# Kernel tuning notes

Measured on AMD Instinct MI355X. Metric: run time of the kernel, lower is better.

## Reference

```python
import jax, jax.numpy as jnp
import numpy as np

NUM_HEADS = 12
EPS = 1e-4


def softmax_kernel(data, proj, is_query):
    # data: [B,H,N,d], proj: [M,d] -> phi: [B,H,N,M]  (Performer softmax-kernel features)
    d = data.shape[-1]
    data_normalizer = d ** -0.25
    ratio = proj.shape[0] ** -0.5
    data_dash = jnp.einsum('bhnd,md->bhnm', data_normalizer * data, proj)
    diag = jnp.sum(data * data, axis=-1, keepdims=True) * 0.5 * (data_normalizer ** 2)
    if is_query:
        m = jnp.max(data_dash, axis=-1, keepdims=True)
    else:
        m = jnp.max(data_dash, axis=(-3, -2, -1), keepdims=True)
    return ratio * (jnp.exp(data_dash - diag - m) + EPS)


def setup_inputs() -> dict:
    key = jax.random.key(0)
    ks = jax.random.split(key, 5)
    B, N, C = 8, 4096, 768
    x = jax.random.normal(ks[0], (B, N, C), dtype=jnp.float32)
    w_qkv = jax.random.normal(ks[1], (3 * C, C), dtype=jnp.float32) * 0.02
    w_proj = jax.random.normal(ks[2], (C, C), dtype=jnp.float32) * 0.02
    b_proj = jnp.zeros((C,), dtype=jnp.float32)
    proj_mat = jax.random.normal(ks[3], (256, C // NUM_HEADS), dtype=jnp.float32)
    return {"x": x, "w_qkv": w_qkv, "w_proj": w_proj, "b_proj": b_proj, "proj_mat": proj_mat}


def reference(x, w_qkv, w_proj, b_proj, proj_mat):
    B, N, C = x.shape
    H = NUM_HEADS
    d = C // H
    qkv = (x @ w_qkv.T).reshape(B, N, 3, H, d).transpose(2, 0, 3, 1, 4)  # [3,B,H,N,d]
    q, k, v = qkv[0], qkv[1], qkv[2]
    q_prime = softmax_kernel(q, proj_mat, is_query=True)   # [B,H,N,M]
    k_prime = softmax_kernel(k, proj_mat, is_query=False)  # [B,H,N,M]
    # non-causal linear attention: out = phi(q) (phi(k)^T v) / (phi(q) sum phi(k))
    k_sum = jnp.sum(k_prime, axis=-2)                       # [B,H,M]
    d_inv = 1.0 / jnp.einsum('bhnm,bhm->bhn', q_prime, k_sum)
    context = jnp.einsum('bhnm,bhnd->bhmd', k_prime, v)     # [B,H,M,d]
    out = jnp.einsum('bhnm,bhmd,bhn->bhnd', q_prime, context, d_inv)
    out = out.transpose(0, 2, 1, 3).reshape(B, N, C)        # b h n d -> b n (h d)
    return out @ w_proj.T + b_proj
```

## Files before the change

kernel.cpp:

```cpp
#include <hip/hip_runtime.h>
#include <hip/hip_bf16.h>

typedef __attribute__((ext_vector_type(4))) float f32x4;
typedef __attribute__((ext_vector_type(8))) short s16x8;
typedef __attribute__((ext_vector_type(4))) float f4v;
typedef __attribute__((ext_vector_type(4))) unsigned short us4;
typedef unsigned short u16;
typedef unsigned int u32;

#define H_ 12
#define NTOK 4096
#define DHEAD 64
#define MFEAT 256
#define CDIM 768

#define NORMALIZER 0.35355339059327373f
#define DIAGSCALE 0.0625f
#define RATIO_ 0.0625f
#define EPS_ 1e-4f
#define DEFER_THR 4.0f

#define MFMA(a, b, c) __builtin_amdgcn_mfma_f32_16x16x32_bf16((a), (b), (c), 0, 0, 0)

__device__ __forceinline__ float bf2f(u16 u) {
  union { float f; u32 v; } x; x.v = ((u32)u) << 16; return x.f;
}
__device__ __forceinline__ u16 f2bf(float f) {
  union { float f; u32 v; } x; x.f = f;
  u32 v = x.v + 0x7FFFu + ((x.v >> 16) & 1u);
  return (u16)(v >> 16);
}
__device__ __forceinline__ u32 fenc(float f) {
  u32 u = __float_as_uint(f);
  return (u & 0x80000000u) ? ~u : (u | 0x80000000u);
}
__device__ __forceinline__ float fdec(u32 k) {
  u32 u = (k & 0x80000000u) ? (k & 0x7fffffffu) : ~k;
  return __uint_as_float(u);
}
__device__ __forceinline__ void glds16(const u16* g, u16* l) {
  __builtin_amdgcn_global_load_lds((const __attribute__((address_space(1))) void*)g,
                                   (__attribute__((address_space(3))) void*)l, 16, 0, 0);
}

__device__ __forceinline__ void st_write64(const u16* stw, u16* dst, long ld, int lane) {
  int r0 = lane >> 3, cc = lane & 7;
#pragma unroll
  for (int c = 0; c < 8; ++c) {
    int row = c * 8 + r0;
    s16x8 v = *(const s16x8*)(stw + row * 72 + cc * 8);
    *(s16x8*)(dst + (long)row * ld + cc * 8) = v;
  }
}

__global__ void cvt_all(const float* __restrict__ x, const float* __restrict__ wq,
                        const float* __restrict__ wp, const float* __restrict__ pj,
                        u16* __restrict__ xb, u16* __restrict__ wqb,
                        u16* __restrict__ wpb, u16* __restrict__ pjb, u32* __restrict__ mk) {
  int b = blockIdx.x;
  if (b == 0 && threadIdx.x < 8) mk[threadIdx.x] = 0u;
  const float* s;
  u16* d;
  int base;
  if (b < 24576)      { s = x;  d = xb;  base = b; }
  else if (b < 26304) { s = wq; d = wqb; base = b - 24576; }
  else if (b < 26880) { s = wp; d = wpb; base = b - 26304; }
  else                { s = pj; d = pjb; base = b - 26880; }
  long i = (long)base * 256 + threadIdx.x;
  f4v v = *(const f4v*)(s + i * 4);
  us4 o;
#pragma unroll
  for (int j = 0; j < 4; ++j) o[j] = f2bf(v[j]);
  *(us4*)(d + i * 4) = o;
}

__global__ __launch_bounds__(256) void k0_qkv(const u16* __restrict__ A, const u16* __restrict__ Bm,
                                              const u16* __restrict__ projb,
                                              u16* __restrict__ qb, u16* __restrict__ kb,
                                              u16* __restrict__ vT, u32* __restrict__ mk) {
  __shared__ u16 smem[4 * 64 * 72];
  u16* lA = smem;
  u16* lB = smem + 8192;
  int tid = threadIdx.x, lane = tid & 63, wid = tid >> 6;
  int p = blockIdx.x + blockIdx.y * 18;
  int r8 = p & 7, q = p >> 3;
  int bx = q % 18;
  int by = (q / 18) * 8 + r8;
  int m0 = by << 7, n0 = bx << 7;
  int wr = (wid >> 1) << 6, wc = (wid & 1) << 6;
  int l15 = lane & 15, lk = lane >> 4;
  int lr = lane >> 3;
  int lu = (lane & 7) ^ lr;
  const u16* Ab = A + (long)m0 * CDIM;
  const u16* Bb = Bm + (long)n0 * CDIM;
  const u16* gA = Ab + (long)(wid * 32 + lr) * CDIM + lu * 8;
  const u16* gB = Bb + (long)(wid * 32 + lr) * CDIM + lu * 8;
  u16* dA = lA + wid * 2048;
  u16* dB = lB + wid * 2048;
  f32x4 acc[4][4];
#pragma unroll
  for (int i = 0; i < 4; ++i)
#pragma unroll
    for (int j = 0; j < 4; ++j) acc[i][j] = (f32x4){0.f, 0.f, 0.f, 0.f};
  for (int k0 = 0; k0 < CDIM; k0 += 64) {
    __syncthreads();
#pragma unroll
    for (int g = 0; g < 4; ++g) {
      glds16(gA + k0 + (long)g * 8 * CDIM, dA + g * 512);
      glds16(gB + k0 + (long)g * 8 * CDIM, dB + g * 512);
    }
    __syncthreads();
#pragma unroll
    for (int ks = 0; ks < 2; ++ks) {
      s16x8 af[4], bv[4];
#pragma unroll
      for (int i = 0; i < 4; ++i) {
        int co = ((ks * 4 + lk) ^ (l15 & 7)) * 8;
        af[i] = *(const s16x8*)(lA + (wr + i * 16 + l15) * 64 + co);
        bv[i] = *(const s16x8*)(lB + (wc + i * 16 + l15) * 64 + co);
      }
#pragma unroll
      for (int i = 0; i < 4; ++i)
#pragma unroll
        for (int j = 0; j < 4; ++j) acc[i][j] = MFMA(af[i], bv[j], acc[i][j]);
    }
  }
  __syncthreads();
  int colbase = n0 + wc;
  int qi = colbase / CDIM;
  int h = (colbase % CDIM) >> 6;
  int rowbase = m0 + wr;
  int b = rowbase >> 12;
  int nloc = rowbase & (NTOK - 1);
  u16* stw = smem + wid * 4608;
  if (qi < 2) {
#pragma unroll
    for (int i = 0; i < 4; ++i)
#pragma unroll
      for (int j = 0; j < 4; ++j)
#pragma unroll
        for (int r = 0; r < 4; ++r)
          stw[(i * 16 + lk * 4 + r) * 72 + j * 16 + l15] = f2bf(acc[i][j][r]);
    u16* dst = (qi == 0 ? qb : kb) + ((long)(b * H_ + h) * NTOK + nloc) * DHEAD;
    st_write64(stw, dst, DHEAD, lane);
    if (qi == 1) {
      float wm = -3.4e38f;
#pragma unroll
      for (int jc = 0; jc < 8; ++jc) {
        s16x8 af2[4][2], bv2[2][2];
#pragma unroll
        for (int ks = 0; ks < 2; ++ks) {
#pragma unroll
          for (int i = 0; i < 4; ++i)
            af2[i][ks] = *(const s16x8*)(stw + (i * 16 + l15) * 72 + ks * 32 + lk * 8);
#pragma unroll
          for (int j2 = 0; j2 < 2; ++j2)
            bv2[j2][ks] = *(const s16x8*)(projb + (long)(jc * 32 + j2 * 16 + l15) * DHEAD + ks * 32 + lk * 8);
        }
        f32x4 dacc[4][2];
#pragma unroll
        for (int i = 0; i < 4; ++i)
#pragma unroll
          for (int j2 = 0; j2 < 2; ++j2) dacc[i][j2] = (f32x4){0.f, 0.f, 0.f, 0.f};
#pragma unroll
        for (int ks = 0; ks < 2; ++ks)
#pragma unroll
          for (int i = 0; i < 4; ++i)
#pragma unroll
            for (int j2 = 0; j2 < 2; ++j2)
              dacc[i][j2] = MFMA(af2[i][ks], bv2[j2][ks], dacc[i][j2]);
#pragma unroll
        for (int i = 0; i < 4; ++i)
#pragma unroll
          for (int j2 = 0; j2 < 2; ++j2)
#pragma unroll
            for (int r = 0; r < 4; ++r) wm = fmaxf(wm, dacc[i][j2][r]);
      }
      wm = fmaxf(wm, __shfl_xor(wm, 1));
      wm = fmaxf(wm, __shfl_xor(wm, 2));
      wm = fmaxf(wm, __shfl_xor(wm, 4));
      wm = fmaxf(wm, __shfl_xor(wm, 8));
      wm = fmaxf(wm, __shfl_xor(wm, 16));
      wm = fmaxf(wm, __shfl_xor(wm, 32));
      if (lane == 0) atomicMax(mk + b, fenc(wm * NORMALIZER));
    }
  } else {
#pragma unroll
    for (int i = 0; i < 4; ++i)
#pragma unroll
      for (int j = 0; j < 4; ++j) {
        us4 w;
#pragma unroll
        for (int r = 0; r < 4; ++r) w[r] = f2bf(acc[i][j][r]);
        *(us4*)(stw + (j * 16 + l15) * 72 + i * 16 + lk * 4) = w;
      }
    u16* dst = vT + (long)(b * H_ + h) * DHEAD * NTOK + nloc;
    st_write64(stw, dst, NTOK, lane);
  }
}

__global__ __launch_bounds__(256) void k3f(const u16* __restrict__ kb, const u16* __restrict__ vT,
                                           const u16* __restrict__ projb, const u32* __restrict__ mk,
                                           float* __restrict__ ctx8, float* __restrict__ kpart) {
  __shared__ u16 smem[4 * 64 * 72];
  int bh = blockIdx.y, nc = blockIdx.x;
  int tid = threadIdx.x, lane = tid & 63, wid = tid >> 6;
  int l15 = lane & 15, lk = lane >> 4;
  int wc = wid << 6;
  float mg = fdec(mk[bh / H_]);
  const u16* Kb = kb + ((long)bh * NTOK + nc * 512) * DHEAD;
  const u16* Vb = vT + (long)bh * DHEAD * NTOK + nc * 512;
  u16* ktw = smem + wid * 4608;
  f32x4 ctxa[4][4];
#pragma unroll
  for (int i = 0; i < 4; ++i)
#pragma unroll
    for (int j = 0; j < 4; ++j) ctxa[i][j] = (f32x4){0.f, 0.f, 0.f, 0.f};
  float cs[4] = {0.f, 0.f, 0.f, 0.f};
  for (int sb = 0; sb < 8; ++sb) {
    const u16* Ksb = Kb + sb * 64 * DHEAD;
    s16x8 a[4][2];
    float ss[4] = {0.f, 0.f, 0.f, 0.f};
#pragma unroll
    for (int i = 0; i < 4; ++i)
#pragma unroll
      for (int ks = 0; ks < 2; ++ks) {
        a[i][ks] = *(const s16x8*)(Ksb + (long)(i * 16 + l15) * DHEAD + ks * 32 + lk * 8);
#pragma unroll
        for (int e = 0; e < 8; ++e) { float f = bf2f((u16)a[i][ks][e]); ss[i] += f * f; }
      }
    float dgv[4];
#pragma unroll
    for (int i = 0; i < 4; ++i) {
      float s = ss[i];
      s += __shfl_xor(s, 16);
      s += __shfl_xor(s, 32);
      dgv[i] = s * DIAGSCALE;
    }
    f32x4 dacc[4][4];
#pragma unroll
    for (int i = 0; i < 4; ++i)
#pragma unroll
      for (int j = 0; j < 4; ++j) dacc[i][j] = (f32x4){0.f, 0.f, 0.f, 0.f};
    __builtin_amdgcn_s_setprio(1);
#pragma unroll
    for (int ks = 0; ks < 2; ++ks)
#pragma unroll
      for (int j = 0; j < 4; ++j) {
        s16x8 pb = *(const s16x8*)(projb + (long)(wc + j * 16 + l15) * DHEAD + ks * 32 + lk * 8);
#pragma unroll
        for (int i = 0; i < 4; ++i) dacc[i][j] = MFMA(a[i][ks], pb, dacc[i][j]);
      }
    __builtin_amdgcn_s_setprio(0);
    float dgr[4][4];
#pragma unroll
    for (int i = 0; i < 4; ++i)
#pragma unroll
      for (int r = 0; r < 4; ++r) dgr[i][r] = __shfl(dgv[i], 4 * lk + r);
#pragma unroll
    for (int i = 0; i < 4; ++i)
#pragma unroll
      for (int j = 0; j < 4; ++j) {
        us4 w;
#pragma unroll
        for (int r = 0; r < 4; ++r) {
          float v = RATIO_ * (__expf(dacc[i][j][r] * NORMALIZER - dgr[i][r] - mg) + EPS_);
          cs[j] += v;
          w[r] = f2bf(v);
        }
        *(us4*)(ktw + (j * 16 + l15) * 72 + i * 16 + lk * 4) = w;
      }
    __builtin_amdgcn_s_setprio(1);
#pragma unroll
    for (int ks = 0; ks < 2; ++ks) {
      s16x8 a2f[4], vb[4];
#pragma unroll
      for (int ii = 0; ii < 4; ++ii)
        a2f[ii] = *(const s16x8*)(ktw + (ii * 16 + l15) * 72 + ks * 32 + lk * 8);
#pragma unroll
      for (int jv = 0; jv < 4; ++jv)
        vb[jv] = *(const s16x8*)(Vb + (long)(jv * 16 + l15) * NTOK + sb * 64 + ks * 32 + lk * 8);
#pragma unroll
      for (int ii = 0; ii < 4; ++ii)
#pragma unroll
        for (int jv = 0; jv < 4; ++jv) ctxa[ii][jv] = MFMA(a2f[ii], vb[jv], ctxa[ii][jv]);
    }
    __builtin_amdgcn_s_setprio(0);
  }
  asm volatile("" ::: "memory");
  float* lf = (float*)ktw;
  float* dstb = ctx8 + (long)(nc * 96 + bh) * (MFEAT * DHEAD);
#pragma unroll
  for (int half = 0; half < 2; ++half) {
#pragma unroll
    for (int jh = 0; jh < 2; ++jh) {
      int jv = half * 2 + jh;
#pragma unroll
      for (int ii = 0; ii < 4; ++ii)
        *(f4v*)(lf + (jh * 16 + l15) * 68 + ii * 16 + lk * 4) =
            (f4v){ctxa[ii][jv][0], ctxa[ii][jv][1], ctxa[ii][jv][2], ctxa[ii][jv][3]};
    }
#pragma unroll
    for (int u = 0; u < 8; ++u) {
      int dd_l = u * 4 + lk;
      f4v v = *(const f4v*)(lf + dd_l * 68 + l15 * 4);
      *(f4v*)(dstb + (long)(half * 32 + dd_l) * MFEAT + wc + l15 * 4) = v;
    }
    asm volatile("" ::: "memory");
  }
#pragma unroll
  for (int j = 0; j < 4; ++j) {
    float s = cs[j];
    s += __shfl_xor(s, 16);
    s += __shfl_xor(s, 32);
    if (lk == 0) kpart[((long)bh * 8 + nc) * MFEAT + wc + j * 16 + l15] = s;
  }
}

__global__ __launch_bounds__(256) void k3b(const float* __restrict__ ctx8, const float* __restrict__ kpart,
                                           u16* __restrict__ baug, float* __restrict__ bsum) {
  int bh = blockIdx.x, y = blockIdx.y;
  int tid = threadIdx.x;
  u16* o = baug + (long)bh * 80 * MFEAT;
  if (y < 4) {
    int dd = y * 16 + (tid >> 4);
    int m0 = (tid & 15) * 16;
    f4v s[4];
#pragma unroll
    for (int e = 0; e < 4; ++e) s[e] = (f4v){0.f, 0.f, 0.f, 0.f};
    for (int c = 0; c < 8; ++c) {
      const float* r = ctx8 + (long)(c * 96 + bh) * (MFEAT * DHEAD) + dd * MFEAT + m0;
#pragma unroll
      for (int e = 0; e < 4; ++e) s[e] += *(const f4v*)(r + e * 4);
    }
    float t = 0.f;
#pragma unroll
    for (int e = 0; e < 4; ++e) {
      us4 w;
#pragma unroll
      for (int q = 0; q < 4; ++q) { t += s[e][q]; w[q] = f2bf(s[e][q]); }
      *(us4*)(o + dd * MFEAT + m0 + e * 4) = w;
    }
    t += __shfl_xor(t, 1); t += __shfl_xor(t, 2); t += __shfl_xor(t, 4); t += __shfl_xor(t, 8);
    if ((tid & 15) == 0) bsum[bh * 80 + dd] = t;
  } else {
    __shared__ float red[4];
    int m = tid;
    float ks = 0.f;
    for (int c = 0; c < 8; ++c) ks += kpart[((long)bh * 8 + c) * MFEAT + m];
    o[64 * MFEAT + m] = f2bf(ks);
    float t = ks;
    t += __shfl_xor(t, 1); t += __shfl_xor(t, 2); t += __shfl_xor(t, 4);
    t += __shfl_xor(t, 8); t += __shfl_xor(t, 16); t += __shfl_xor(t, 32);
    if ((m & 63) == 0) red[m >> 6] = t;
    __syncthreads();
    if (m == 0) bsum[bh * 80 + 64] = red[0] + red[1] + red[2] + red[3];
    for (int dd = 65; dd < 80; ++dd) o[dd * MFEAT + m] = 0;
    if (m < 15) bsum[bh * 80 + 65 + m] = 0.f;
  }
}

__global__ __launch_bounds__(256) void k2q5(const u16* __restrict__ qb, const u16* __restrict__ projb,
                                            const u16* __restrict__ baug, const float* __restrict__ bsum,
                                            u16* __restrict__ attn) {
  __shared__ u16 smem[4 * 64 * 72];
  int bh = blockIdx.y;
  int b = bh / H_, h = bh % H_;
  int tid = threadIdx.x, lane = tid & 63, wid = tid >> 6;
  int l15 = lane & 15, lk = lane >> 4;
  int tb = blockIdx.x * 256 + wid * 64;
  const u16* Aq = qb + ((long)bh * NTOK + tb) * DHEAD;
  const u16* Bb = baug + (long)bh * 80 * MFEAT;
  u16* qTw = smem + wid * 4608;

  s16x8 a2[4][2];
  float ssv[4] = {0.f, 0.f, 0.f, 0.f};
#pragma unroll
  for (int i = 0; i < 4; ++i)
#pragma unroll
    for (int ks = 0; ks < 2; ++ks) {
      a2[i][ks] = *(const s16x8*)(Aq + (long)(i * 16 + l15) * DHEAD + ks * 32 + lk * 8);
#pragma unroll
      for (int e = 0; e < 8; ++e) { float f = bf2f((u16)a2[i][ks][e]); ssv[i] += f * f; }
    }
  float dgv[4];
#pragma unroll
  for (int i = 0; i < 4; ++i) {
    float s = ssv[i];
    s += __shfl_xor(s, 16);
    s += __shfl_xor(s, 32);
    dgv[i] = s * DIAGSCALE;
  }
  float rm[4] = {-3.4e38f, -3.4e38f, -3.4e38f, -3.4e38f};
  float tm[4] = {-3.4e38f, -3.4e38f, -3.4e38f, -3.4e38f};
  f32x4 oacc[5][4];
#pragma unroll
  for (int jo = 0; jo < 5; ++jo)
#pragma unroll
    for (int i = 0; i < 4; ++i) oacc[jo][i] = (f32x4){0.f, 0.f, 0.f, 0.f};

  for (int c = 0; c < 8; ++c) {
    s16x8 pb[2][2];
#pragma unroll
    for (int j = 0; j < 2; ++j)
#pragma unroll
      for (int ks = 0; ks < 2; ++ks)
        pb[j][ks] = *(const s16x8*)(projb + (long)(c * 32 + j * 16 + l15) * DHEAD + ks * 32 + lk * 8);
    f32x4 dacc[2][4];
#pragma unroll
    for (int j = 0; j < 2; ++j)
#pragma unroll
      for (int i = 0; i < 4; ++i) dacc[j][i] = (f32x4){0.f, 0.f, 0.f, 0.f};
    __builtin_amdgcn_s_setprio(1);
#pragma unroll
    for (int ks = 0; ks < 2; ++ks)
#pragma unroll
      for (int j = 0; j < 2; ++j)
#pragma unroll
        for (int i = 0; i < 4; ++i) dacc[j][i] = MFMA(pb[j][ks], a2[i][ks], dacc[j][i]);
    __builtin_amdgcn_s_setprio(0);
#pragma unroll
    for (int i = 0; i < 4; ++i) {
      float cm = dacc[0][i][0];
      cm = fmaxf(cm, dacc[0][i][1]); cm = fmaxf(cm, dacc[0][i][2]); cm = fmaxf(cm, dacc[0][i][3]);
      cm = fmaxf(cm, dacc[1][i][0]); cm = fmaxf(cm, dacc[1][i][1]);
      cm = fmaxf(cm, dacc[1][i][2]); cm = fmaxf(cm, dacc[1][i][3]);
      cm = fmaxf(cm, __shfl_xor(cm, 16));
      cm = fmaxf(cm, __shfl_xor(cm, 32));
      tm[i] = fmaxf(tm[i], cm);
      if (__any((cm - rm[i]) * NORMALIZER > DEFER_THR)) {
        float rn = fmaxf(rm[i], cm);
        float fsc = __expf((rm[i] - rn) * NORMALIZER);
#pragma unroll
        for (int jo = 0; jo < 5; ++jo) oacc[jo][i] *= fsc;
        rm[i] = rn;
      }
    }
#pragma unroll
    for (int i = 0; i < 4; ++i) {
      float dm = dgv[i] + rm[i] * NORMALIZER;
#pragma unroll
      for (int j = 0; j < 2; ++j) {
        us4 w;
#pragma unroll
        for (int r = 0; r < 4; ++r)
          w[r] = f2bf(RATIO_ * __expf(dacc[j][i][r] * NORMALIZER - dm));
        *(us4*)(qTw + (i * 16 + l15) * 40 + j * 16 + lk * 4) = w;
      }
    }
    s16x8 bB[5], qf[4];
#pragma unroll
    for (int jo = 0; jo < 5; ++jo)
      bB[jo] = *(const s16x8*)(Bb + (long)(jo * 16 + l15) * MFEAT + c * 32 + lk * 8);
#pragma unroll
    for (int i = 0; i < 4; ++i)
      qf[i] = *(const s16x8*)(qTw + (i * 16 + l15) * 40 + lk * 8);
    __builtin_amdgcn_s_setprio(1);
#pragma unroll
    for (int jo = 0; jo < 5; ++jo)
#pragma unroll
      for (int i = 0; i < 4; ++i) oacc[jo][i] = MFMA(bB[jo], qf[i], oacc[jo][i]);
    __builtin_amdgcn_s_setprio(0);
  }
  float lamv[4];
#pragma unroll
  for (int i = 0; i < 4; ++i) lamv[i] = __expf((tm[i] - rm[i]) * NORMALIZER);
#pragma unroll
  for (int jo = 0; jo < 5; ++jo) {
    f4v bs = *(const f4v*)(bsum + (long)bh * 80 + jo * 16 + lk * 4);
#pragma unroll
    for (int i = 0; i < 4; ++i)
#pragma unroll
      for (int r = 0; r < 4; ++r) oacc[jo][i][r] += (RATIO_ * EPS_) * bs[r] * lamv[i];
  }
  u16* stw = qTw;
#pragma unroll
  for (int i = 0; i < 4; ++i) {
    float dn = __shfl(oacc[4][i][0], l15);
    float inv = 1.0f / dn;
#pragma unroll
    for (int jo = 0; jo < 4; ++jo) {
      us4 w;
#pragma unroll
      for (int r = 0; r < 4; ++r) w[r] = f2bf(oacc[jo][i][r] * inv);
      *(us4*)(stw + (i * 16 + l15) * 72 + jo * 16 + lk * 4) = w;
    }
  }
  u16* dst = attn + ((long)b * NTOK + tb) * CDIM + h * DHEAD;
  st_write64(stw, dst, CDIM, lane);
}

__global__ __launch_bounds__(256) void k6_proj(const u16* __restrict__ A, const u16* __restrict__ Bm,
                                               const float* __restrict__ bproj, float* __restrict__ out) {
  __shared__ u16 smem[16384];
  u16* lA = smem;
  u16* lB = smem + 8192;
  int tid = threadIdx.x, lane = tid & 63, wid = tid >> 6;
  int p = blockIdx.x + blockIdx.y * 6;
  int r8 = p & 7, q = p >> 3;
  int bx = q % 6;
  int by = (q / 6) * 8 + r8;
  int m0 = by << 7, n0 = bx << 7;
  int wr = (wid >> 1) << 6, wc = (wid & 1) << 6;
  int l15 = lane & 15, lk = lane >> 4;
  int lr = lane >> 3;
  int lu = (lane & 7) ^ lr;
  const u16* Ab = A + (long)m0 * CDIM;
  const u16* Bb = Bm + (long)n0 * CDIM;
  const u16* gA = Ab + (long)(wid * 32 + lr) * CDIM + lu * 8;
  const u16* gB = Bb + (long)(wid * 32 + lr) * CDIM + lu * 8;
  u16* dA = lA + wid * 2048;
  u16* dB = lB + wid * 2048;
  f32x4 acc[4][4];
#pragma unroll
  for (int i = 0; i < 4; ++i)
#pragma unroll
    for (int j = 0; j < 4; ++j) acc[i][j] = (f32x4){0.f, 0.f, 0.f, 0.f};
  for (int k0 = 0; k0 < CDIM; k0 += 64) {
    __syncthreads();
#pragma unroll
    for (int g = 0; g < 4; ++g) {
      glds16(gA + k0 + (long)g * 8 * CDIM, dA + g * 512);
      glds16(gB + k0 + (long)g * 8 * CDIM, dB + g * 512);
    }
    __syncthreads();
#pragma unroll
    for (int ks = 0; ks < 2; ++ks) {
      s16x8 af[4], bv[4];
#pragma unroll
      for (int i = 0; i < 4; ++i) {
        int co = ((ks * 4 + lk) ^ (l15 & 7)) * 8;
        af[i] = *(const s16x8*)(lA + (wr + i * 16 + l15) * 64 + co);
        bv[i] = *(const s16x8*)(lB + (wc + i * 16 + l15) * 64 + co);
      }
#pragma unroll
      for (int i = 0; i < 4; ++i)
#pragma unroll
        for (int j = 0; j < 4; ++j) acc[i][j] = MFMA(af[i], bv[j], acc[i][j]);
    }
  }
  float bpv[4];
#pragma unroll
  for (int j = 0; j < 4; ++j) bpv[j] = bproj[n0 + wc + j * 16 + l15];
#pragma unroll
  for (int i = 0; i < 4; ++i)
#pragma unroll
    for (int j = 0; j < 4; ++j)
#pragma unroll
      for (int r = 0; r < 4; ++r) {
        long row = m0 + wr + i * 16 + lk * 4 + r;
        int col = n0 + wc + j * 16 + l15;
        out[row * CDIM + col] = acc[i][j][r] + bpv[j];
      }
}

extern "C" void kernel_launch(void* const* d_in, const int* in_sizes, int n_in,
                              void* d_out, int out_size, void* d_ws, size_t ws_size,
                              hipStream_t stream) {
  const float* x = (const float*)d_in[0];
  const float* w_qkv = (const float*)d_in[1];
  const float* w_proj = (const float*)d_in[2];
  const float* b_proj = (const float*)d_in[3];
  const float* proj = (const float*)d_in[4];
  float* out = (float*)d_out;

  char* p = (char*)d_ws;
  auto take = [&](size_t bytes) {
    char* r = p;
    p += (bytes + 255) & ~(size_t)255;
    return r;
  };
  u16* xb = (u16*)take(32768UL * 768 * 2);
  u16* wqkvb = (u16*)take(2304UL * 768 * 2);
  u16* wprojb = (u16*)take(768UL * 768 * 2);
  u16* projb = (u16*)take(256UL * 64 * 2);
  u16* qb = (u16*)take(96UL * 4096 * 64 * 2);
  u16* kb = (u16*)take(96UL * 4096 * 64 * 2);
  u16* vT = (u16*)take(96UL * 64 * 4096 * 2);
  float* kpart = (float*)take(96UL * 8 * 256 * 4);
  u32* mk = (u32*)take(256);
  u16* baug = (u16*)take(96UL * 80 * 256 * 2);
  float* bsum = (float*)take(96UL * 80 * 4);
  float* ctx8 = (float*)xb;
  u16* attn = kb;

  cvt_all<<<26896, 256, 0, stream>>>(x, w_qkv, w_proj, proj, xb, wqkvb, wprojb, projb, mk);
  k0_qkv<<<dim3(18, 256), 256, 0, stream>>>(xb, wqkvb, projb, qb, kb, vT, mk);
  k3f<<<dim3(8, 96), 256, 0, stream>>>(kb, vT, projb, mk, ctx8, kpart);
  k3b<<<dim3(96, 5), 256, 0, stream>>>(ctx8, kpart, baug, bsum);
  k2q5<<<dim3(16, 96), 256, 0, stream>>>(qb, projb, baug, bsum, attn);
  k6_proj<<<dim3(6, 256), 256, 0, stream>>>(attn, wprojb, b_proj, out);
}
```

Baseline: 455.9 us.

## Replace global key-max prepass with online per-wave running max and rescaling

Drops the extra projection GEMM and atomicMax that k0_qkv ran on K to find the global per-batch max. k3f now keeps a running max per wave, rescaling its partial context and key sums only when the max jumps past a threshold. It also records per-chunk maxima and V column sums. k3b recombines the partials with exp scale factors and adds the EPS term analytically through the V sums. This removes redundant MFMA work and the atomic from the QKV GEMM epilogue, at the cost of extra reduction logic, more buffers, and possible numeric drift when a rescale is deferred.

```diff
diff --git a/kernel.cpp b/kernel.cpp
--- a/kernel.cpp
+++ b/kernel.cpp
@@ -30,14 +30,6 @@
   u32 v = x.v + 0x7FFFu + ((x.v >> 16) & 1u);
   return (u16)(v >> 16);
 }
-__device__ __forceinline__ u32 fenc(float f) {
-  u32 u = __float_as_uint(f);
-  return (u & 0x80000000u) ? ~u : (u | 0x80000000u);
-}
-__device__ __forceinline__ float fdec(u32 k) {
-  u32 u = (k & 0x80000000u) ? (k & 0x7fffffffu) : ~k;
-  return __uint_as_float(u);
-}
 __device__ __forceinline__ void glds16(const u16* g, u16* l) {
   __builtin_amdgcn_global_load_lds((const __attribute__((address_space(1))) void*)g,
                                    (__attribute__((address_space(3))) void*)l, 16, 0, 0);
@@ -56,9 +48,8 @@
 __global__ void cvt_all(const float* __restrict__ x, const float* __restrict__ wq,
                         const float* __restrict__ wp, const float* __restrict__ pj,
                         u16* __restrict__ xb, u16* __restrict__ wqb,
-                        u16* __restrict__ wpb, u16* __restrict__ pjb, u32* __restrict__ mk) {
+                        u16* __restrict__ wpb, u16* __restrict__ pjb) {
   int b = blockIdx.x;
-  if (b == 0 && threadIdx.x < 8) mk[threadIdx.x] = 0u;
   const float* s;
   u16* d;
   int base;
@@ -75,9 +66,8 @@
 }
 
 __global__ __launch_bounds__(256) void k0_qkv(const u16* __restrict__ A, const u16* __restrict__ Bm,
-                                              const u16* __restrict__ projb,
                                               u16* __restrict__ qb, u16* __restrict__ kb,
-                                              u16* __restrict__ vT, u32* __restrict__ mk) {
+                                              u16* __restrict__ vT) {
   __shared__ u16 smem[4 * 64 * 72];
   u16* lA = smem;
   u16* lB = smem + 8192;
@@ -143,47 +133,6 @@
           stw[(i * 16 + lk * 4 + r) * 72 + j * 16 + l15] = f2bf(acc[i][j][r]);
     u16* dst = (qi == 0 ? qb : kb) + ((long)(b * H_ + h) * NTOK + nloc) * DHEAD;
     st_write64(stw, dst, DHEAD, lane);
-    if (qi == 1) {
-      float wm = -3.4e38f;
-#pragma unroll
-      for (int jc = 0; jc < 8; ++jc) {
-        s16x8 af2[4][2], bv2[2][2];
-#pragma unroll
-        for (int ks = 0; ks < 2; ++ks) {
-#pragma unroll
-          for (int i = 0; i < 4; ++i)
-            af2[i][ks] = *(const s16x8*)(stw + (i * 16 + l15) * 72 + ks * 32 + lk * 8);
-#pragma unroll
-          for (int j2 = 0; j2 < 2; ++j2)
-            bv2[j2][ks] = *(const s16x8*)(projb + (long)(jc * 32 + j2 * 16 + l15) * DHEAD + ks * 32 + lk * 8);
-        }
-        f32x4 dacc[4][2];
-#pragma unroll
-        for (int i = 0; i < 4; ++i)
-#pragma unroll
-          for (int j2 = 0; j2 < 2; ++j2) dacc[i][j2] = (f32x4){0.f, 0.f, 0.f, 0.f};
-#pragma unroll
-        for (int ks = 0; ks < 2; ++ks)
-#pragma unroll
-          for (int i = 0; i < 4; ++i)
-#pragma unroll
-            for (int j2 = 0; j2 < 2; ++j2)
-              dacc[i][j2] = MFMA(af2[i][ks], bv2[j2][ks], dacc[i][j2]);
-#pragma unroll
-        for (int i = 0; i < 4; ++i)
-#pragma unroll
-          for (int j2 = 0; j2 < 2; ++j2)
-#pragma unroll
-            for (int r = 0; r < 4; ++r) wm = fmaxf(wm, dacc[i][j2][r]);
-      }
-      wm = fmaxf(wm, __shfl_xor(wm, 1));
-      wm = fmaxf(wm, __shfl_xor(wm, 2));
-      wm = fmaxf(wm, __shfl_xor(wm, 4));
-      wm = fmaxf(wm, __shfl_xor(wm, 8));
-      wm = fmaxf(wm, __shfl_xor(wm, 16));
-      wm = fmaxf(wm, __shfl_xor(wm, 32));
-      if (lane == 0) atomicMax(mk + b, fenc(wm * NORMALIZER));
-    }
   } else {
 #pragma unroll
     for (int i = 0; i < 4; ++i)
@@ -200,14 +149,15 @@
 }
 
 __global__ __launch_bounds__(256) void k3f(const u16* __restrict__ kb, const u16* __restrict__ vT,
-                                           const u16* __restrict__ projb, const u32* __restrict__ mk,
-                                           float* __restrict__ ctx8, float* __restrict__ kpart) {
+                                           const u16* __restrict__ projb,
+                                           float* __restrict__ ctx8, float* __restrict__ kpart,
+                                           float* __restrict__ tmbuf, float* __restrict__ rmbuf,
+                                           float* __restrict__ vsumb) {
   __shared__ u16 smem[4 * 64 * 72];
   int bh = blockIdx.y, nc = blockIdx.x;
   int tid = threadIdx.x, lane = tid & 63, wid = tid >> 6;
   int l15 = lane & 15, lk = lane >> 4;
   int wc = wid << 6;
-  float mg = fdec(mk[bh / H_]);
   const u16* Kb = kb + ((long)bh * NTOK + nc * 512) * DHEAD;
   const u16* Vb = vT + (long)bh * DHEAD * NTOK + nc * 512;
   u16* ktw = smem + wid * 4608;
@@ -217,6 +167,8 @@
 #pragma unroll
     for (int j = 0; j < 4; ++j) ctxa[i][j] = (f32x4){0.f, 0.f, 0.f, 0.f};
   float cs[4] = {0.f, 0.f, 0.f, 0.f};
+  float rm = -3.4e38f, tm = -3.4e38f;
+  float vsacc[4] = {0.f, 0.f, 0.f, 0.f};
   for (int sb = 0; sb < 8; ++sb) {
     const u16* Ksb = Kb + sb * 64 * DHEAD;
     s16x8 a[4][2];
@@ -252,6 +204,31 @@
         for (int i = 0; i < 4; ++i) dacc[i][j] = MFMA(a[i][ks], pb, dacc[i][j]);
       }
     __builtin_amdgcn_s_setprio(0);
+    float cm = -3.4e38f;
+#pragma unroll
+    for (int i = 0; i < 4; ++i)
+#pragma unroll
+      for (int j = 0; j < 4; ++j)
+#pragma unroll
+        for (int r = 0; r < 4; ++r) cm = fmaxf(cm, dacc[i][j][r]);
+    cm = fmaxf(cm, __shfl_xor(cm, 1));
+    cm = fmaxf(cm, __shfl_xor(cm, 2));
+    cm = fmaxf(cm, __shfl_xor(cm, 4));
+    cm = fmaxf(cm, __shfl_xor(cm, 8));
+    cm = fmaxf(cm, __shfl_xor(cm, 16));
+    cm = fmaxf(cm, __shfl_xor(cm, 32));
+    tm = fmaxf(tm, cm);
+    if ((cm - rm) * NORMALIZER > DEFER_THR) {
+      float fsc = __expf((rm - cm) * NORMALIZER);
+#pragma unroll
+      for (int ii = 0; ii < 4; ++ii)
+#pragma unroll
+        for (int jv = 0; jv < 4; ++jv) ctxa[ii][jv] *= fsc;
+#pragma unroll
+      for (int j = 0; j < 4; ++j) cs[j] *= fsc;
+      rm = cm;
+    }
+    float rmN = rm * NORMALIZER;
     float dgr[4][4];
 #pragma unroll
     for (int i = 0; i < 4; ++i)
@@ -264,7 +241,7 @@
         us4 w;
 #pragma unroll
         for (int r = 0; r < 4; ++r) {
-          float v = RATIO_ * (__expf(dacc[i][j][r] * NORMALIZER - dgr[i][r] - mg) + EPS_);
+          float v = __expf(dacc[i][j][r] * NORMALIZER - dgr[i][r] - rmN);
           cs[j] += v;
           w[r] = f2bf(v);
         }
@@ -280,6 +257,12 @@
 #pragma unroll
       for (int jv = 0; jv < 4; ++jv)
         vb[jv] = *(const s16x8*)(Vb + (long)(jv * 16 + l15) * NTOK + sb * 64 + ks * 32 + lk * 8);
+      if (wid == 0) {
+#pragma unroll
+        for (int jv = 0; jv < 4; ++jv)
+#pragma unroll
+          for (int e = 0; e < 8; ++e) vsacc[jv] += bf2f((u16)vb[jv][e]);
+      }
 #pragma unroll
       for (int ii = 0; ii < 4; ++ii)
 #pragma unroll
@@ -315,39 +298,86 @@
     s += __shfl_xor(s, 32);
     if (lk == 0) kpart[((long)bh * 8 + nc) * MFEAT + wc + j * 16 + l15] = s;
   }
+  if (lane == 0) {
+    tmbuf[bh * 32 + nc * 4 + wid] = tm;
+    rmbuf[bh * 32 + nc * 4 + wid] = rm;
+  }
+  if (wid == 0) {
+#pragma unroll
+    for (int jv = 0; jv < 4; ++jv) {
+      float s = vsacc[jv];
+      s += __shfl_xor(s, 16);
+      s += __shfl_xor(s, 32);
+      if (lk == 0) vsumb[((long)bh * 8 + nc) * 64 + jv * 16 + l15] = s;
+    }
+  }
 }
 
 __global__ __launch_bounds__(256) void k3b(const float* __restrict__ ctx8, const float* __restrict__ kpart,
+                                           const float* __restrict__ tmbuf, const float* __restrict__ rmbuf,
+                                           const float* __restrict__ vsumb,
                                            u16* __restrict__ baug, float* __restrict__ bsum) {
+  __shared__ float red[4];
+  __shared__ float mgs;
   int bh = blockIdx.x, y = blockIdx.y;
-  int tid = threadIdx.x;
+  int tid = threadIdx.x, lane = tid & 63, wid4 = tid >> 6;
+  int b = bh / H_;
+  float ml = -3.4e38f;
+  for (int i = tid; i < 384; i += 256) ml = fmaxf(ml, tmbuf[b * 384 + i]);
+  ml = fmaxf(ml, __shfl_xor(ml, 1));
+  ml = fmaxf(ml, __shfl_xor(ml, 2));
+  ml = fmaxf(ml, __shfl_xor(ml, 4));
+  ml = fmaxf(ml, __shfl_xor(ml, 8));
+  ml = fmaxf(ml, __shfl_xor(ml, 16));
+  ml = fmaxf(ml, __shfl_xor(ml, 32));
+  if (lane == 0) red[wid4] = ml;
+  __syncthreads();
+  if (tid == 0) mgs = fmaxf(fmaxf(red[0], red[1]), fmaxf(red[2], red[3]));
+  __syncthreads();
+  float mg = mgs;
   u16* o = baug + (long)bh * 80 * MFEAT;
   if (y < 4) {
     int dd = y * 16 + (tid >> 4);
     int m0 = (tid & 15) * 16;
+    int qd = m0 >> 6;
+    float scale[8];
+#pragma unroll
+    for (int c = 0; c < 8; ++c)
+      scale[c] = __expf((rmbuf[bh * 32 + c * 4 + qd] - mg) * NORMALIZER);
     f4v s[4];
 #pragma unroll
     for (int e = 0; e < 4; ++e) s[e] = (f4v){0.f, 0.f, 0.f, 0.f};
     for (int c = 0; c < 8; ++c) {
       const float* r = ctx8 + (long)(c * 96 + bh) * (MFEAT * DHEAD) + dd * MFEAT + m0;
 #pragma unroll
-      for (int e = 0; e < 4; ++e) s[e] += *(const f4v*)(r + e * 4);
-    }
+      for (int e = 0; e < 4; ++e) s[e] += scale[c] * (*(const f4v*)(r + e * 4));
+    }
+    float vs = 0.f;
+#pragma unroll
+    for (int c = 0; c < 8; ++c) vs += vsumb[((long)bh * 8 + c) * 64 + dd];
+    float epsb = RATIO_ * EPS_ * vs;
     float t = 0.f;
 #pragma unroll
     for (int e = 0; e < 4; ++e) {
       us4 w;
 #pragma unroll
-      for (int q = 0; q < 4; ++q) { t += s[e][q]; w[q] = f2bf(s[e][q]); }
+      for (int q = 0; q < 4; ++q) {
+        float val = RATIO_ * s[e][q] + epsb;
+        t += val;
+        w[q] = f2bf(val);
+      }
       *(us4*)(o + dd * MFEAT + m0 + e * 4) = w;
     }
     t += __shfl_xor(t, 1); t += __shfl_xor(t, 2); t += __shfl_xor(t, 4); t += __shfl_xor(t, 8);
     if ((tid & 15) == 0) bsum[bh * 80 + dd] = t;
   } else {
-    __shared__ float red[4];
     int m = tid;
+    int qd = m >> 6;
     float ks = 0.f;
-    for (int c = 0; c < 8; ++c) ks += kpart[((long)bh * 8 + c) * MFEAT + m];
+#pragma unroll
+    for (int c = 0; c < 8; ++c)
+      ks += __expf((rmbuf[bh * 32 + c * 4 + qd] - mg) * NORMALIZER) * kpart[((long)bh * 8 + c) * MFEAT + m];
+    ks = RATIO_ * ks + RATIO_ * EPS_ * 4096.0f;
     o[64 * MFEAT + m] = f2bf(ks);
     float t = ks;
     t += __shfl_xor(t, 1); t += __shfl_xor(t, 2); t += __shfl_xor(t, 4);
@@ -578,16 +608,18 @@
   u16* kb = (u16*)take(96UL * 4096 * 64 * 2);
   u16* vT = (u16*)take(96UL * 64 * 4096 * 2);
   float* kpart = (float*)take(96UL * 8 * 256 * 4);
-  u32* mk = (u32*)take(256);
   u16* baug = (u16*)take(96UL * 80 * 256 * 2);
   float* bsum = (float*)take(96UL * 80 * 4);
+  float* tmbuf = (float*)take(96UL * 32 * 4);
+  float* rmbuf = (float*)take(96UL * 32 * 4);
+  float* vsumb = (float*)take(96UL * 8 * 64 * 4);
   float* ctx8 = (float*)xb;
   u16* attn = kb;
 
-  cvt_all<<<26896, 256, 0, stream>>>(x, w_qkv, w_proj, proj, xb, wqkvb, wprojb, projb, mk);
-  k0_qkv<<<dim3(18, 256), 256, 0, stream>>>(xb, wqkvb, projb, qb, kb, vT, mk);
-  k3f<<<dim3(8, 96), 256, 0, stream>>>(kb, vT, projb, mk, ctx8, kpart);
-  k3b<<<dim3(96, 5), 256, 0, stream>>>(ctx8, kpart, baug, bsum);
+  cvt_all<<<26896, 256, 0, stream>>>(x, w_qkv, w_proj, proj, xb, wqkvb, wprojb, projb);
+  k0_qkv<<<dim3(18, 256), 256, 0, stream>>>(xb, wqkvb, qb, kb, vT);
+  k3f<<<dim3(8, 96), 256, 0, stream>>>(kb, vT, projb, ctx8, kpart, tmbuf, rmbuf, vsumb);
+  k3b<<<dim3(96, 5), 256, 0, stream>>>(ctx8, kpart, tmbuf, rmbuf, vsumb, baug, bsum);
   k2q5<<<dim3(16, 96), 256, 0, stream>>>(qb, projb, baug, bsum, attn);
   k6_proj<<<dim3(6, 256), 256, 0, stream>>>(attn, wprojb, b_proj, out);
 }
```

Result: faster. 415.6 us (-8.8%).
